# Kernel optimization log

Hardware: AMD Instinct MI355X
Metric: run time of the kernel (lower is better)

The kernel has to match this reference:

```python
import jax, jax.numpy as jnp
import numpy as np

CIN = (512, 1024, 512, 256, 256, 256)
S = (64, 32, 16, 8, 4, 2)
P = 7  # corr_size
B = 8
CH = [P * P + c // 8 for c in CIN]  # lstm state channels per level


def conv3x3(x, w, b):
    y = jax.lax.conv_general_dilated(x, w, (1, 1), ((1, 1), (1, 1)),
                                     dimension_numbers=('NCHW', 'OIHW', 'NCHW'))
    return y + b[None, :, None, None]


def spatial_corr(f1, f2, patch=P):
    # corr[b, di*patch+dj, y, x] = sum_c f1[b,c,y,x] * f2[b,c, y+di-r, x+dj-r]
    r = patch // 2
    Bn, C, H, W = f1.shape
    f2p = jnp.pad(f2, ((0, 0), (0, 0), (r, r), (r, r)))
    outs = [jnp.sum(f1 * f2p[:, :, di:di + H, dj:dj + W], axis=1)
            for di in range(patch) for dj in range(patch)]
    return jnp.stack(outs, axis=1)  # (B, patch*patch, H, W)


def setup_inputs() -> dict:
    key = jax.random.key(0)
    ks = iter(jax.random.split(key, 200))
    d = {}
    for i, (c, s) in enumerate(zip(CIN, S)):
        ch = CH[i]
        d[f'x{i}'] = jax.random.normal(next(ks), (B, c, s, s), jnp.float32)
        d[f'xp{i}'] = jax.random.normal(next(ks), (B, c, s, s), jnp.float32)
        d[f'h{i}'] = jax.random.normal(next(ks), (B, ch, s, s), jnp.float32)
        d[f'c{i}'] = jax.random.normal(next(ks), (B, ch, s, s), jnp.float32)
        d[f'sw{i}'] = jax.random.normal(next(ks), (c // 8, c, 3, 3), jnp.float32) / np.sqrt(c * 9.0)
        d[f'sb{i}'] = jnp.zeros((c // 8,), jnp.float32)
        d[f'lw{i}'] = jax.random.normal(next(ks), (4 * ch, 2 * ch, 3, 3), jnp.float32) / np.sqrt(2 * ch * 9.0)
        d[f'lb{i}'] = jnp.zeros((4 * ch,), jnp.float32)
    return d


def _forward(xs, xps, hs, cs, sws, sbs, lws, lbs):
    h_next, c_next, corrs = [], [], []
    for i in range(len(CIN)):
        summary = jax.nn.relu(conv3x3(xs[i], sws[i], sbs[i]))            # (B, C/8, s, s)
        cf = jax.nn.leaky_relu(spatial_corr(xs[i], xps[i]), 0.01)        # (B, P*P, s, s)
        corrs.append(cf)
        lstm_in = jnp.concatenate([summary, cf, hs[i]], axis=1)          # (B, 2*ch, s, s)
        cx = conv3x3(lstm_in, lws[i], lbs[i])                            # (B, 4*ch, s, s)
        ci, cfg, co, cg = jnp.split(cx, 4, axis=1)
        ig = jax.nn.sigmoid(ci)
        fg = jax.nn.sigmoid(cfg)
        og = jax.nn.sigmoid(co)
        gg = jnp.tanh(cg)
        cn = fg * cs[i] + ig * gg
        hn = og * jnp.tanh(cn)
        h_next.append(hn)
        c_next.append(cn)
    return tuple(h_next + c_next + corrs)


def reference(x0, x1, x2, x3, x4, x5,
              xp0, xp1, xp2, xp3, xp4, xp5,
              h0, h1, h2, h3, h4, h5,
              c0, c1, c2, c3, c4, c5,
              sw0, sw1, sw2, sw3, sw4, sw5,
              sb0, sb1, sb2, sb3, sb4, sb5,
              lw0, lw1, lw2, lw3, lw4, lw5,
              lb0, lb1, lb2, lb3, lb4, lb5):
    xs = [x0, x1, x2, x3, x4, x5]
    xps = [xp0, xp1, xp2, xp3, xp4, xp5]
    hs = [h0, h1, h2, h3, h4, h5]
    cs = [c0, c1, c2, c3, c4, c5]
    sws = [sw0, sw1, sw2, sw3, sw4, sw5]
    sbs = [sb0, sb1, sb2, sb3, sb4, sb5]
    lws = [lw0, lw1, lw2, lw3, lw4, lw5]
    lbs = [lb0, lb1, lb2, lb3, lb4, lb5]
    return _forward(xs, xps, hs, cs, sws, sbs, lws, lbs)
```

## Files before the change

### kernel.cpp

```cpp
#include <hip/hip_runtime.h>
#include <math.h>

typedef _Float16 f16;
typedef _Float16 f16x8 __attribute__((ext_vector_type(8)));
typedef float f32x4 __attribute__((ext_vector_type(4)));

__device__ __forceinline__ float sigmoidf_(float x) { return 1.0f / (1.0f + expf(-x)); }

#define NB 8

__device__ __forceinline__ void decode_swz(int p, int Mtiles, int& mtile, int& nt) {
  if ((Mtiles & 7) == 0) {
    int mch = Mtiles >> 3;
    int c = p & 7, inner = p >> 3;
    nt = inner / mch;
    mtile = c * mch + (inner - nt * mch);
  } else {
    mtile = p % Mtiles;
    nt = p / Mtiles;
  }
}

__global__ void k_nchw2nhwc(const float* __restrict__ in, f16* __restrict__ out,
                            int C, int S, int Cpad, int coff, int Wp, int pad) {
  __shared__ float tile[16][17];
  int xt = blockIdx.x;
  int ct = blockIdx.y;
  int by = blockIdx.z;
  int b = by / S, y = by % S;
  int x0 = xt * 16, c0 = ct * 16;
  int tx = threadIdx.x & 15, tc = threadIdx.x >> 4;
  float v = 0.f;
  if (c0 + tc < C && x0 + tx < S)
    v = in[(((size_t)b * C + c0 + tc) * S + y) * S + x0 + tx];
  tile[tc][tx] = v;
  __syncthreads();
  int tcc = threadIdx.x & 15;
  int txx = threadIdx.x >> 4;
  if (c0 + tcc < C && x0 + txx < S)
    out[(((size_t)b * Wp + y + pad) * Wp + (x0 + txx + pad)) * Cpad + coff + c0 + tcc]
        = (f16)tile[tcc][txx];
}

__global__ void k_wlstm(const float* __restrict__ w, f16* __restrict__ wt,
                        int CH, int CH2, int Jpad, int Cpad) {
  int idx = blockIdx.x * blockDim.x + threadIdx.x;
  int total = 9 * 4 * Jpad * Cpad;
  if (idx >= total) return;
  int ci = idx % Cpad; int t = idx / Cpad;
  int j = t % Jpad; t /= Jpad;
  int g = t % 4; int kk = t / 4;
  float v = 0.f;
  if (j < CH && ci < CH2)
    v = w[((size_t)(g * CH + j) * CH2 + ci) * 9 + kk];
  wt[idx] = (f16)v;
}

__global__ void k_wsum(const float* __restrict__ w, f16* __restrict__ wt,
                       int C8, int C, int Npad, int Cpad) {
  int idx = blockIdx.x * blockDim.x + threadIdx.x;
  int total = 9 * Npad * Cpad;
  if (idx >= total) return;
  int ci = idx % Cpad; int t = idx / Cpad;
  int co = t % Npad; int kk = t / Npad;
  float v = 0.f;
  if (co < C8 && ci < C)
    v = w[((size_t)co * C + ci) * 9 + kk];
  wt[idx] = (f16)v;
}

__global__ void __launch_bounds__(256)
k_conv_gemm(const f16* __restrict__ A,
            const f16* __restrict__ Wt,
            const float* __restrict__ bias,
            f16* __restrict__ D,
            int S, int lS, int CpadX, int CpadL, int C8, int Npad, int M) {
  int w = threadIdx.x >> 6;
  int lane = threadIdx.x & 63;
  int quad = lane >> 4, r = lane & 15;
  int Mtiles = (M + 63) >> 6;
  int mtile, ntile;
  decode_swz(blockIdx.x, Mtiles, mtile, ntile);
  int Sp = S + 2;
  size_t abase[4];
#pragma unroll
  for (int s = 0; s < 4; s++) {
    int m = mtile * 64 + s * 16 + r;
    if (m >= M) m = M - 1;
    int b = m >> (2 * lS);
    int rem = m & ((1 << (2 * lS)) - 1);
    int y = rem >> lS, x = rem & ((1 << lS) - 1);
    abase[s] = (((size_t)b * Sp + y) * Sp + x) * CpadX + quad * 8;
  }
  f32x4 acc[4][4] = {};
  int n0 = ntile * 64;
  int KB = CpadX >> 5;
  int T = 9 * KB;
  int T4 = (T + 3) >> 2;
  int it = w * T4;
  int itEnd = (T < it + T4) ? T : it + T4;
  int nIt = itEnd - it;
  int cb = it / 9;
  int kk = it - cb * 9;

#define CG_LOAD(AF, BF) do { \
    int ky_ = kk / 3, kx_ = kk - 3 * ky_; \
    size_t aoff_ = ((size_t)(ky_ * Sp + kx_)) * CpadX + (size_t)cb * 32; \
    const f16* wp_ = Wt + ((size_t)kk * Npad + n0 + r) * CpadX + quad * 8 + (size_t)cb * 32; \
    _Pragma("unroll") for (int s_ = 0; s_ < 4; s_++) \
      AF[s_] = *(const f16x8*)(A + abase[s_] + aoff_); \
    _Pragma("unroll") for (int t_ = 0; t_ < 4; t_++) \
      BF[t_] = *(const f16x8*)(wp_ + (size_t)t_ * 16 * CpadX); \
  } while (0)
#define CG_ADV() do { kk++; if (kk == 9) { kk = 0; cb++; } } while (0)
#define CG_MF(AF, BF) do { \
    _Pragma("unroll") for (int s_ = 0; s_ < 4; s_++) \
    _Pragma("unroll") for (int t_ = 0; t_ < 4; t_++) \
      acc[s_][t_] = __builtin_amdgcn_mfma_f32_16x16x32_f16(AF[s_], BF[t_], acc[s_][t_], 0, 0, 0); \
  } while (0)

  {
    f16x8 a0[4], b0[4], a1[4], b1[4];
    if (nIt > 0) {
      CG_LOAD(a0, b0); CG_ADV();
      int rem = nIt - 1;
      while (rem >= 2) {
        CG_LOAD(a1, b1); CG_ADV();
        CG_MF(a0, b0);
        CG_LOAD(a0, b0); CG_ADV();
        CG_MF(a1, b1);
        rem -= 2;
      }
      if (rem == 1) { CG_LOAD(a1, b1); CG_MF(a0, b0); CG_MF(a1, b1); }
      else { CG_MF(a0, b0); }
    }
  }
#undef CG_LOAD
#undef CG_ADV
#undef CG_MF

  __shared__ f32x4 red[4][2][4][64];
#pragma unroll
  for (int sh = 0; sh < 2; sh++)
#pragma unroll
    for (int t = 0; t < 4; t++)
      red[w][sh][t][lane] = acc[sh][t];
  __syncthreads();
  f32x4 accR[4];
  if (w < 2) {
#pragma unroll
    for (int t = 0; t < 4; t++)
      accR[t] = red[0][w][t][lane] + red[1][w][t][lane] + red[2][w][t][lane] + red[3][w][t][lane];
  }
  __syncthreads();
#pragma unroll
  for (int sh = 0; sh < 2; sh++)
#pragma unroll
    for (int t = 0; t < 4; t++)
      red[w][sh][t][lane] = acc[2 + sh][t];
  __syncthreads();
  if (w >= 2) {
#pragma unroll
    for (int t = 0; t < 4; t++)
      accR[t] = red[0][w - 2][t][lane] + red[1][w - 2][t][lane] + red[2][w - 2][t][lane] + red[3][w - 2][t][lane];
  }

#pragma unroll
  for (int i = 0; i < 4; i++) {
    int m = mtile * 64 + w * 16 + quad * 4 + i;
    if (m >= M) continue;
    int b = m >> (2 * lS);
    int rem = m & ((1 << (2 * lS)) - 1);
    int y = rem >> lS, x = rem & ((1 << lS) - 1);
    size_t dbase = (((size_t)b * Sp + y + 1) * Sp + (x + 1)) * CpadL;
#pragma unroll
    for (int t = 0; t < 4; t++) {
      int co = n0 + t * 16 + r;
      if (co < C8) {
        float v = accR[t][i] + bias[co];
        D[dbase + co] = (f16)fmaxf(v, 0.f);
      }
    }
  }
}

__global__ void __launch_bounds__(256)
k_lstm_gemm(const f16* __restrict__ A,
            const f16* __restrict__ Wt,
            const float* __restrict__ lb,
            const float* __restrict__ cprev,
            float* __restrict__ hout, float* __restrict__ cout,
            int S, int lS, int CpadL, int CH, int Jpad, int M) {
  int w = threadIdx.x >> 6;
  int lane = threadIdx.x & 63;
  int quad = lane >> 4, r = lane & 15;
  int Mtiles = (M + 63) >> 6;
  int mtile, jt;
  decode_swz(blockIdx.x, Mtiles, mtile, jt);
  int j0 = jt * 16;
  int Sp = S + 2;
  size_t abase[4];
#pragma unroll
  for (int s = 0; s < 4; s++) {
    int m = mtile * 64 + s * 16 + r;
    if (m >= M) m = M - 1;
    int b = m >> (2 * lS);
    int rem = m & ((1 << (2 * lS)) - 1);
    int y = rem >> lS, x = rem & ((1 << lS) - 1);
    abase[s] = (((size_t)b * Sp + y) * Sp + x) * CpadL + quad * 8;
  }
  f32x4 acc[4][4] = {};
  int KB = CpadL >> 5;
  int T = 9 * KB;
  int T4 = (T + 3) >> 2;
  int it = w * T4;
  int itEnd = (T < it + T4) ? T : it + T4;
  int nIt = itEnd - it;
  int cb = it / 9;
  int kk = it - cb * 9;

#define LG_LOAD(AF, BF) do { \
    int ky_ = kk / 3, kx_ = kk - 3 * ky_; \
    size_t aoff_ = ((size_t)(ky_ * Sp + kx_)) * CpadL + (size_t)cb * 32; \
    const f16* wp_ = Wt + (((size_t)kk * 4) * Jpad + j0 + r) * CpadL + quad * 8 + (size_t)cb * 32; \
    _Pragma("unroll") for (int s_ = 0; s_ < 4; s_++) \
      AF[s_] = *(const f16x8*)(A + abase[s_] + aoff_); \
    _Pragma("unroll") for (int g_ = 0; g_ < 4; g_++) \
      BF[g_] = *(const f16x8*)(wp_ + (size_t)g_ * Jpad * CpadL); \
  } while (0)
#define LG_ADV() do { kk++; if (kk == 9) { kk = 0; cb++; } } while (0)
#define LG_MF(AF, BF) do { \
    _Pragma("unroll") for (int s_ = 0; s_ < 4; s_++) \
    _Pragma("unroll") for (int g_ = 0; g_ < 4; g_++) \
      acc[s_][g_] = __builtin_amdgcn_mfma_f32_16x16x32_f16(AF[s_], BF[g_], acc[s_][g_], 0, 0, 0); \
  } while (0)

  {
    f16x8 a0[4], b0[4], a1[4], b1[4];
    if (nIt > 0) {
      LG_LOAD(a0, b0); LG_ADV();
      int rem = nIt - 1;
      while (rem >= 2) {
        LG_LOAD(a1, b1); LG_ADV();
        LG_MF(a0, b0);
        LG_LOAD(a0, b0); LG_ADV();
        LG_MF(a1, b1);
        rem -= 2;
      }
      if (rem == 1) { LG_LOAD(a1, b1); LG_MF(a0, b0); LG_MF(a1, b1); }
      else { LG_MF(a0, b0); }
    }
  }
#undef LG_LOAD
#undef LG_ADV
#undef LG_MF

  __shared__ f32x4 red[4][2][4][64];
#pragma unroll
  for (int sh = 0; sh < 2; sh++)
#pragma unroll
    for (int g = 0; g < 4; g++)
      red[w][sh][g][lane] = acc[sh][g];
  __syncthreads();
  f32x4 accR[4];
  if (w < 2) {
#pragma unroll
    for (int g = 0; g < 4; g++)
      accR[g] = red[0][w][g][lane] + red[1][w][g][lane] + red[2][w][g][lane] + red[3][w][g][lane];
  }
  __syncthreads();
#pragma unroll
  for (int sh = 0; sh < 2; sh++)
#pragma unroll
    for (int g = 0; g < 4; g++)
      red[w][sh][g][lane] = acc[2 + sh][g];
  __syncthreads();
  if (w >= 2) {
#pragma unroll
    for (int g = 0; g < 4; g++)
      accR[g] = red[0][w - 2][g][lane] + red[1][w - 2][g][lane] + red[2][w - 2][g][lane] + red[3][w - 2][g][lane];
  }

  int j = j0 + r;
  if (j >= CH) return;
  float bi = lb[j];
  float bf_ = lb[CH + j];
  float bo = lb[2 * CH + j];
  float bg = lb[3 * CH + j];
#pragma unroll
  for (int i = 0; i < 4; i++) {
    int m = mtile * 64 + w * 16 + quad * 4 + i;
    if (m >= M) continue;
    int b = m >> (2 * lS);
    int rem = m & ((1 << (2 * lS)) - 1);
    int y = rem >> lS, x = rem & ((1 << lS) - 1);
    size_t o = (((size_t)b * CH + j) * S + y) * S + x;
    float ig = sigmoidf_(accR[0][i] + bi);
    float fg = sigmoidf_(accR[1][i] + bf_);
    float og = sigmoidf_(accR[2][i] + bo);
    float gg = tanhf(accR[3][i] + bg);
    float cn = fg * cprev[o] + ig * gg;
    hout[o] = og * tanhf(cn);
    cout[o] = cn;
  }
}

__global__ void k_corr(const float* __restrict__ f1, const float* __restrict__ f2,
                       float* __restrict__ corr_out, f16* __restrict__ D,
                       int C, int S, int CpadL, int C8) {
  int idx = blockIdx.x * blockDim.x + threadIdx.x;
  int total = NB * 49 * S * S;
  if (idx >= total) return;
  int px = idx % S; int t = idx / S;
  int py = t % S; t /= S;
  int d = t % 49; int b = t / 49;
  int qy = py + d / 7 - 3;
  int qx = px + d % 7 - 3;

  float acc = 0.f;
  if (qy >= 0 && qy < S && qx >= 0 && qx < S) {
    const float* p1 = f1 + ((size_t)b * C * S + py) * S + px;
    const float* p2 = f2 + ((size_t)b * C * S + qy) * S + qx;
    size_t cs = (size_t)S * S;
    for (int ci = 0; ci < C; ci++) {
      acc += p1[(size_t)ci * cs] * p2[(size_t)ci * cs];
    }
  }
  float lr = (acc > 0.f) ? acc : 0.01f * acc;
  corr_out[idx] = lr;
  int Sp = S + 2;
  D[(((size_t)b * Sp + py + 1) * Sp + (px + 1)) * CpadL + C8 + d] = (f16)lr;
}

template<int S>
__global__ void __launch_bounds__(256)
k_corr_mfma(const f16* __restrict__ A,
            const f16* __restrict__ A2,
            float* __restrict__ corr_out,
            f16* __restrict__ D,
            int C, int CpadL, int C8) {
  constexpr int XT = S / 16;
  constexpr int Sp = S + 2, Sq = S + 6;
  int nb = gridDim.x;
  int eb = (blockIdx.x % 8) * (nb / 8) + blockIdx.x / 8;
  int wid = eb * 4 + (threadIdx.x >> 6);
  int lane = threadIdx.x & 63;
  int quad = lane >> 4, r = lane & 15;
  int xt = wid % XT; int t1 = wid / XT;
  int y = t1 % S; int b = t1 / S;
  int x0 = xt * 16;

  const f16* pa = A + (((size_t)b * Sp + (y + 1)) * Sp + (x0 + r + 1)) * C + quad * 8;
  int xs1 = x0 + 16 + r; if (xs1 > S + 5) xs1 = S + 5;
  size_t off0 = (size_t)(x0 + r) * C + (size_t)quad * 8;
  size_t off1 = (size_t)xs1 * C + (size_t)quad * 8;
  const f16* pb = A2 + ((size_t)b * Sq + y) * Sq * C;

  f32x4 acc[7][2] = {};
  for (int cb = 0; cb < C; cb += 32) {
    f16x8 af = *(const f16x8*)(pa + cb);
#pragma unroll
    for (int dyo = 0; dyo < 7; dyo++) {
      const f16* pr = pb + (size_t)dyo * Sq * C + cb;
      f16x8 b0 = *(const f16x8*)(pr + off0);
      f16x8 b1 = *(const f16x8*)(pr + off1);
      acc[dyo][0] = __builtin_amdgcn_mfma_f32_16x16x32_f16(af, b0, acc[dyo][0], 0, 0, 0);
      acc[dyo][1] = __builtin_amdgcn_mfma_f32_16x16x32_f16(af, b1, acc[dyo][1], 0, 0, 0);
    }
  }
#pragma unroll
  for (int dyo = 0; dyo < 7; dyo++) {
#pragma unroll
    for (int t = 0; t < 2; t++) {
#pragma unroll
      for (int i = 0; i < 4; i++) {
        int ml = quad * 4 + i;
        int dxo = r - ml + t * 16;
        if (dxo < 0 || dxo > 6) continue;
        float v = acc[dyo][t][i];
        float lr = (v > 0.f) ? v : 0.01f * v;
        int d = dyo * 7 + dxo;
        int x = x0 + ml;
        corr_out[(((size_t)b * 49 + d) * S + y) * S + x] = lr;
        D[(((size_t)b * Sp + y + 1) * Sp + (x + 1)) * CpadL + C8 + d] = (f16)lr;
      }
    }
  }
}

extern "C" void kernel_launch(void* const* d_in, const int* in_sizes, int n_in,
                              void* d_out, int out_size, void* d_ws, size_t ws_size,
                              hipStream_t stream) {
  (void)in_sizes; (void)n_in; (void)out_size; (void)ws_size;
  static const int CINa[6] = {512, 1024, 512, 256, 256, 256};
  static const int Sa[6]   = {64, 32, 16, 8, 4, 2};
  static const int lSa[6]  = {6, 5, 4, 3, 2, 1};
  static const int CHa[6]  = {113, 177, 113, 81, 81, 81};
  static const int CpadLa[6] = {256, 384, 256, 192, 192, 192};
  static const int Jpada[6]  = {128, 192, 128, 96, 96, 96};
  const int B = 8;

  size_t h_off[6], c_off[6], corr_off[6];
  size_t off = 0;
  for (int i = 0; i < 6; i++) { h_off[i] = off;    off += (size_t)B * CHa[i] * Sa[i] * Sa[i]; }
  for (int i = 0; i < 6; i++) { c_off[i] = off;    off += (size_t)B * CHa[i] * Sa[i] * Sa[i]; }
  for (int i = 0; i < 6; i++) { corr_off[i] = off; off += (size_t)B * 49 * Sa[i] * Sa[i]; }

  float* out = (float*)d_out;
  char* ws = (char*)d_ws;
  const size_t offA = 0;
  const size_t offD = 37748736;
  const size_t offWs = offD + 18874368;
  const size_t offWl = offWs + 3145728;
  const size_t offA2 = offWl + 6291456;

  for (int i = 0; i < 6; i++) {
    const float* x  = (const float*)d_in[8 * i + 0];
    const float* xp = (const float*)d_in[8 * i + 1];
    const float* h  = (const float*)d_in[8 * i + 2];
    const float* c  = (const float*)d_in[8 * i + 3];
    const float* sw = (const float*)d_in[8 * i + 4];
    const float* sb = (const float*)d_in[8 * i + 5];
    const float* lw = (const float*)d_in[8 * i + 6];
    const float* lb = (const float*)d_in[8 * i + 7];
    int C = CINa[i], S = Sa[i], lS = lSa[i], CH = CHa[i], C8 = C / 8;
    int CH2 = 2 * CH, CpadL = CpadLa[i], Jpad = Jpada[i];
    int Sp = S + 2;
    int Npad = (C8 + 63) / 64 * 64;
    int M = B * S * S;
    int Mtiles = (M + 63) / 64;

    f16* Abuf = (f16*)(ws + offA);
    f16* Dbuf = (f16*)(ws + offD);
    f16* Wsum = (f16*)(ws + offWs);
    f16* Wlstm = (f16*)(ws + offWl);
    f16* A2buf = (f16*)(ws + offA2);

    size_t sizeA = (size_t)B * Sp * Sp * C * 2;
    size_t sizeD = (size_t)B * Sp * Sp * CpadL * 2;
    hipMemsetAsync(Abuf, 0, sizeA, stream);
    hipMemsetAsync(Dbuf, 0, sizeD, stream);

    {
      dim3 g((S + 15) / 16, (C + 15) / 16, B * S);
      k_nchw2nhwc<<<g, 256, 0, stream>>>(x, Abuf, C, S, C, 0, Sp, 1);
    }
    {
      int tot = 9 * Npad * C;
      k_wsum<<<(tot + 255) / 256, 256, 0, stream>>>(sw, Wsum, C8, C, Npad, C);
    }
    {
      k_conv_gemm<<<Mtiles * (Npad / 64), 256, 0, stream>>>(Abuf, Wsum, sb, Dbuf,
                                                            S, lS, C, CpadL, C8, Npad, M);
    }
    if (i < 3) {
      int Sq = S + 6;
      size_t sizeA2 = (size_t)B * Sq * Sq * C * 2;
      hipMemsetAsync(A2buf, 0, sizeA2, stream);
      {
        dim3 g((S + 15) / 16, (C + 15) / 16, B * S);
        k_nchw2nhwc<<<g, 256, 0, stream>>>(xp, A2buf, C, S, C, 0, Sq, 3);
      }
      int blocks = B * S * (S / 16) / 4;
      if (i == 0)
        k_corr_mfma<64><<<blocks, 256, 0, stream>>>(Abuf, A2buf, out + corr_off[i], Dbuf,
                                                    C, CpadL, C8);
      else if (i == 1)
        k_corr_mfma<32><<<blocks, 256, 0, stream>>>(Abuf, A2buf, out + corr_off[i], Dbuf,
                                                    C, CpadL, C8);
      else
        k_corr_mfma<16><<<blocks, 256, 0, stream>>>(Abuf, A2buf, out + corr_off[i], Dbuf,
                                                    C, CpadL, C8);
    } else {
      int tot = B * 49 * S * S;
      k_corr<<<(tot + 255) / 256, 256, 0, stream>>>(x, xp, out + corr_off[i], Dbuf,
                                                    C, S, CpadL, C8);
    }
    {
      dim3 g((S + 15) / 16, (CH + 15) / 16, B * S);
      k_nchw2nhwc<<<g, 256, 0, stream>>>(h, Dbuf, CH, S, CpadL, C8 + 49, Sp, 1);
    }
    {
      int tot = 9 * 4 * Jpad * CpadL;
      k_wlstm<<<(tot + 255) / 256, 256, 0, stream>>>(lw, Wlstm, CH, CH2, Jpad, CpadL);
    }
    {
      k_lstm_gemm<<<Mtiles * (Jpad / 16), 256, 0, stream>>>(Dbuf, Wlstm, lb, c,
                                                            out + h_off[i], out + c_off[i],
                                                            S, lS, CpadL, CH, Jpad, M);
    }
  }
}
```

Measured before the change: 1.656 ms.

## Use channel-blocked activation and weight layouts, drop split-K reduction in conv GEMMs

Activations move from NHWC to a channel-blocked layout (32-channel blocks, each a padded spatial plane), and weights are repacked into 16x32 tiles, so each MFMA fragment load reads a contiguous chunk. The conv and LSTM GEMMs switch from four waves splitting K with a shared-memory reduction to each wave owning 32 rows of a 128-row M tile over the full K range. This removes the LDS reduction and its barriers. In exchange the grid has half as many blocks per level, which can lower occupancy on the small levels, and each wave now runs the whole K loop alone.

New measurement: 1.682 ms. Within noise of the previous version (+1.5%).

```diff
diff --git a/kernel.cpp b/kernel.cpp
--- a/kernel.cpp
+++ b/kernel.cpp
@@ -37,19 +37,26 @@
   __syncthreads();
   int tcc = threadIdx.x & 15;
   int txx = threadIdx.x >> 4;
-  if (c0 + tcc < C && x0 + txx < S)
-    out[(((size_t)b * Wp + y + pad) * Wp + (x0 + txx + pad)) * Cpad + coff + c0 + tcc]
-        = (f16)tile[tcc][txx];
+  if (c0 + tcc < C && x0 + txx < S) {
+    int c = coff + c0 + tcc;
+    out[((((size_t)b * (Cpad >> 5) + (c >> 5)) * Wp + (y + pad)) * Wp + (x0 + txx + pad)) * 32
+        + (c & 31)] = (f16)tile[tcc][txx];
+  }
 }
 
 __global__ void k_wlstm(const float* __restrict__ w, f16* __restrict__ wt,
                         int CH, int CH2, int Jpad, int Cpad) {
   int idx = blockIdx.x * blockDim.x + threadIdx.x;
-  int total = 9 * 4 * Jpad * Cpad;
+  int JB16 = Jpad >> 4, KBL = Cpad >> 5;
+  int total = 9 * 4 * JB16 * KBL * 512;
   if (idx >= total) return;
-  int ci = idx % Cpad; int t = idx / Cpad;
-  int j = t % Jpad; t /= Jpad;
-  int g = t % 4; int kk = t / 4;
+  int e = idx & 31;
+  int jj = (idx >> 5) & 15;
+  int t = idx >> 9;
+  int cb = t % KBL; t /= KBL;
+  int jb = t % JB16; t /= JB16;
+  int g = t & 3; int kk = t >> 2;
+  int j = jb * 16 + jj, ci = cb * 32 + e;
   float v = 0.f;
   if (j < CH && ci < CH2)
     v = w[((size_t)(g * CH + j) * CH2 + ci) * 9 + kk];
@@ -59,10 +66,15 @@
 __global__ void k_wsum(const float* __restrict__ w, f16* __restrict__ wt,
                        int C8, int C, int Npad, int Cpad) {
   int idx = blockIdx.x * blockDim.x + threadIdx.x;
-  int total = 9 * Npad * Cpad;
+  int NB16 = Npad >> 4, KBX = Cpad >> 5;
+  int total = 9 * NB16 * KBX * 512;
   if (idx >= total) return;
-  int ci = idx % Cpad; int t = idx / Cpad;
-  int co = t % Npad; int kk = t / Npad;
+  int e = idx & 31;
+  int nn = (idx >> 5) & 15;
+  int t = idx >> 9;
+  int cb = t % KBX; t /= KBX;
+  int nb = t % NB16; int kk = t / NB16;
+  int co = nb * 16 + nn, ci = cb * 32 + e;
   float v = 0.f;
   if (co < C8 && ci < C)
     v = w[((size_t)co * C + ci) * 9 + kk];
@@ -78,107 +90,79 @@
   int w = threadIdx.x >> 6;
   int lane = threadIdx.x & 63;
   int quad = lane >> 4, r = lane & 15;
-  int Mtiles = (M + 63) >> 6;
+  int KBX = CpadX >> 5, KBL = CpadL >> 5, NB16 = Npad >> 4;
+  int Mt = (M + 127) >> 7;
   int mtile, ntile;
-  decode_swz(blockIdx.x, Mtiles, mtile, ntile);
+  decode_swz(blockIdx.x, Mt, mtile, ntile);
+  int nb0 = ntile * 4;
   int Sp = S + 2;
-  size_t abase[4];
-#pragma unroll
-  for (int s = 0; s < 4; s++) {
-    int m = mtile * 64 + s * 16 + r;
+  size_t pbase[2];
+#pragma unroll
+  for (int s = 0; s < 2; s++) {
+    int m = mtile * 128 + w * 32 + s * 16 + r;
     if (m >= M) m = M - 1;
     int b = m >> (2 * lS);
     int rem = m & ((1 << (2 * lS)) - 1);
     int y = rem >> lS, x = rem & ((1 << lS) - 1);
-    abase[s] = (((size_t)b * Sp + y) * Sp + x) * CpadX + quad * 8;
-  }
-  f32x4 acc[4][4] = {};
-  int n0 = ntile * 64;
-  int KB = CpadX >> 5;
-  int T = 9 * KB;
-  int T4 = (T + 3) >> 2;
-  int it = w * T4;
-  int itEnd = (T < it + T4) ? T : it + T4;
-  int nIt = itEnd - it;
-  int cb = it / 9;
-  int kk = it - cb * 9;
+    pbase[s] = (((size_t)b * KBX * Sp + y) * Sp + x) * 32 + quad * 8;
+  }
+  size_t wlane = ((size_t)r << 5) + quad * 8;
+  size_t tstep = ((size_t)KBX) << 9;
+  f32x4 acc[2][4] = {};
+  int T = 9 * KBX;
+  int cb = 0, kk = 0;
 
 #define CG_LOAD(AF, BF) do { \
     int ky_ = kk / 3, kx_ = kk - 3 * ky_; \
-    size_t aoff_ = ((size_t)(ky_ * Sp + kx_)) * CpadX + (size_t)cb * 32; \
-    const f16* wp_ = Wt + ((size_t)kk * Npad + n0 + r) * CpadX + quad * 8 + (size_t)cb * 32; \
-    _Pragma("unroll") for (int s_ = 0; s_ < 4; s_++) \
-      AF[s_] = *(const f16x8*)(A + abase[s_] + aoff_); \
+    size_t aoff_ = ((size_t)cb * Sp * Sp + ky_ * Sp + kx_) * 32; \
+    size_t wb_ = (((size_t)(kk * NB16 + nb0) * KBX + cb) << 9) + wlane; \
+    AF[0] = *(const f16x8*)(A + pbase[0] + aoff_); \
+    AF[1] = *(const f16x8*)(A + pbase[1] + aoff_); \
     _Pragma("unroll") for (int t_ = 0; t_ < 4; t_++) \
-      BF[t_] = *(const f16x8*)(wp_ + (size_t)t_ * 16 * CpadX); \
+      BF[t_] = *(const f16x8*)(Wt + wb_ + (size_t)t_ * tstep); \
   } while (0)
 #define CG_ADV() do { kk++; if (kk == 9) { kk = 0; cb++; } } while (0)
 #define CG_MF(AF, BF) do { \
-    _Pragma("unroll") for (int s_ = 0; s_ < 4; s_++) \
+    _Pragma("unroll") for (int s_ = 0; s_ < 2; s_++) \
     _Pragma("unroll") for (int t_ = 0; t_ < 4; t_++) \
       acc[s_][t_] = __builtin_amdgcn_mfma_f32_16x16x32_f16(AF[s_], BF[t_], acc[s_][t_], 0, 0, 0); \
   } while (0)
 
   {
-    f16x8 a0[4], b0[4], a1[4], b1[4];
-    if (nIt > 0) {
+    f16x8 a0[2], b0[4], a1[2], b1[4];
+    CG_LOAD(a0, b0); CG_ADV();
+    int rem = T - 1;
+    while (rem >= 2) {
+      CG_LOAD(a1, b1); CG_ADV();
+      CG_MF(a0, b0);
       CG_LOAD(a0, b0); CG_ADV();
-      int rem = nIt - 1;
-      while (rem >= 2) {
-        CG_LOAD(a1, b1); CG_ADV();
-        CG_MF(a0, b0);
-        CG_LOAD(a0, b0); CG_ADV();
-        CG_MF(a1, b1);
-        rem -= 2;
-      }
-      if (rem == 1) { CG_LOAD(a1, b1); CG_MF(a0, b0); CG_MF(a1, b1); }
-      else { CG_MF(a0, b0); }
-    }
+      CG_MF(a1, b1);
+      rem -= 2;
+    }
+    if (rem == 1) { CG_LOAD(a1, b1); CG_MF(a0, b0); CG_MF(a1, b1); }
+    else { CG_MF(a0, b0); }
   }
 #undef CG_LOAD
 #undef CG_ADV
 #undef CG_MF
 
-  __shared__ f32x4 red[4][2][4][64];
-#pragma unroll
-  for (int sh = 0; sh < 2; sh++)
-#pragma unroll
-    for (int t = 0; t < 4; t++)
-      red[w][sh][t][lane] = acc[sh][t];
-  __syncthreads();
-  f32x4 accR[4];
-  if (w < 2) {
-#pragma unroll
-    for (int t = 0; t < 4; t++)
-      accR[t] = red[0][w][t][lane] + red[1][w][t][lane] + red[2][w][t][lane] + red[3][w][t][lane];
-  }
-  __syncthreads();
-#pragma unroll
-  for (int sh = 0; sh < 2; sh++)
-#pragma unroll
-    for (int t = 0; t < 4; t++)
-      red[w][sh][t][lane] = acc[2 + sh][t];
-  __syncthreads();
-  if (w >= 2) {
-#pragma unroll
-    for (int t = 0; t < 4; t++)
-      accR[t] = red[0][w - 2][t][lane] + red[1][w - 2][t][lane] + red[2][w - 2][t][lane] + red[3][w - 2][t][lane];
-  }
-
-#pragma unroll
-  for (int i = 0; i < 4; i++) {
-    int m = mtile * 64 + w * 16 + quad * 4 + i;
-    if (m >= M) continue;
-    int b = m >> (2 * lS);
-    int rem = m & ((1 << (2 * lS)) - 1);
-    int y = rem >> lS, x = rem & ((1 << lS) - 1);
-    size_t dbase = (((size_t)b * Sp + y + 1) * Sp + (x + 1)) * CpadL;
-#pragma unroll
-    for (int t = 0; t < 4; t++) {
-      int co = n0 + t * 16 + r;
-      if (co < C8) {
-        float v = accR[t][i] + bias[co];
-        D[dbase + co] = (f16)fmaxf(v, 0.f);
+#pragma unroll
+  for (int s = 0; s < 2; s++) {
+#pragma unroll
+    for (int i = 0; i < 4; i++) {
+      int m = mtile * 128 + w * 32 + s * 16 + quad * 4 + i;
+      if (m >= M) continue;
+      int b = m >> (2 * lS);
+      int rem = m & ((1 << (2 * lS)) - 1);
+      int y = rem >> lS, x = rem & ((1 << lS) - 1);
+#pragma unroll
+      for (int t = 0; t < 4; t++) {
+        int co = (nb0 + t) * 16 + r;
+        if (co < C8) {
+          float v = acc[s][t][i] + bias[co];
+          D[((((size_t)b * KBL + (co >> 5)) * Sp + (y + 1)) * Sp + (x + 1)) * 32 + (co & 31)]
+              = (f16)fmaxf(v, 0.f);
+        }
       }
     }
   }
@@ -194,114 +178,85 @@
   int w = threadIdx.x >> 6;
   int lane = threadIdx.x & 63;
   int quad = lane >> 4, r = lane & 15;
-  int Mtiles = (M + 63) >> 6;
+  int KBL = CpadL >> 5, JB16 = Jpad >> 4;
+  int Mt = (M + 127) >> 7;
   int mtile, jt;
-  decode_swz(blockIdx.x, Mtiles, mtile, jt);
-  int j0 = jt * 16;
+  decode_swz(blockIdx.x, Mt, mtile, jt);
   int Sp = S + 2;
-  size_t abase[4];
-#pragma unroll
-  for (int s = 0; s < 4; s++) {
-    int m = mtile * 64 + s * 16 + r;
+  size_t pbase[2];
+#pragma unroll
+  for (int s = 0; s < 2; s++) {
+    int m = mtile * 128 + w * 32 + s * 16 + r;
     if (m >= M) m = M - 1;
     int b = m >> (2 * lS);
     int rem = m & ((1 << (2 * lS)) - 1);
     int y = rem >> lS, x = rem & ((1 << lS) - 1);
-    abase[s] = (((size_t)b * Sp + y) * Sp + x) * CpadL + quad * 8;
-  }
-  f32x4 acc[4][4] = {};
-  int KB = CpadL >> 5;
-  int T = 9 * KB;
-  int T4 = (T + 3) >> 2;
-  int it = w * T4;
-  int itEnd = (T < it + T4) ? T : it + T4;
-  int nIt = itEnd - it;
-  int cb = it / 9;
-  int kk = it - cb * 9;
+    pbase[s] = (((size_t)b * KBL * Sp + y) * Sp + x) * 32 + quad * 8;
+  }
+  size_t wlane = ((size_t)r << 5) + quad * 8;
+  size_t gstep = ((size_t)JB16 * KBL) << 9;
+  f32x4 acc[2][4] = {};
+  int T = 9 * KBL;
+  int cb = 0, kk = 0;
 
 #define LG_LOAD(AF, BF) do { \
     int ky_ = kk / 3, kx_ = kk - 3 * ky_; \
-    size_t aoff_ = ((size_t)(ky_ * Sp + kx_)) * CpadL + (size_t)cb * 32; \
-    const f16* wp_ = Wt + (((size_t)kk * 4) * Jpad + j0 + r) * CpadL + quad * 8 + (size_t)cb * 32; \
-    _Pragma("unroll") for (int s_ = 0; s_ < 4; s_++) \
-      AF[s_] = *(const f16x8*)(A + abase[s_] + aoff_); \
+    size_t aoff_ = ((size_t)cb * Sp * Sp + ky_ * Sp + kx_) * 32; \
+    size_t wb_ = (((size_t)(kk * 4 * JB16 + jt) * KBL + cb) << 9) + wlane; \
+    AF[0] = *(const f16x8*)(A + pbase[0] + aoff_); \
+    AF[1] = *(const f16x8*)(A + pbase[1] + aoff_); \
     _Pragma("unroll") for (int g_ = 0; g_ < 4; g_++) \
-      BF[g_] = *(const f16x8*)(wp_ + (size_t)g_ * Jpad * CpadL); \
+      BF[g_] = *(const f16x8*)(Wt + wb_ + (size_t)g_ * gstep); \
   } while (0)
 #define LG_ADV() do { kk++; if (kk == 9) { kk = 0; cb++; } } while (0)
 #define LG_MF(AF, BF) do { \
-    _Pragma("unroll") for (int s_ = 0; s_ < 4; s_++) \
+    _Pragma("unroll") for (int s_ = 0; s_ < 2; s_++) \
     _Pragma("unroll") for (int g_ = 0; g_ < 4; g_++) \
       acc[s_][g_] = __builtin_amdgcn_mfma_f32_16x16x32_f16(AF[s_], BF[g_], acc[s_][g_], 0, 0, 0); \
   } while (0)
 
   {
-    f16x8 a0[4], b0[4], a1[4], b1[4];
-    if (nIt > 0) {
+    f16x8 a0[2], b0[4], a1[2], b1[4];
+    LG_LOAD(a0, b0); LG_ADV();
+    int rem = T - 1;
+    while (rem >= 2) {
+      LG_LOAD(a1, b1); LG_ADV();
+      LG_MF(a0, b0);
       LG_LOAD(a0, b0); LG_ADV();
-      int rem = nIt - 1;
-      while (rem >= 2) {
-        LG_LOAD(a1, b1); LG_ADV();
-        LG_MF(a0, b0);
-        LG_LOAD(a0, b0); LG_ADV();
-        LG_MF(a1, b1);
-        rem -= 2;
-      }
-      if (rem == 1) { LG_LOAD(a1, b1); LG_MF(a0, b0); LG_MF(a1, b1); }
-      else { LG_MF(a0, b0); }
-    }
+      LG_MF(a1, b1);
+      rem -= 2;
+    }
+    if (rem == 1) { LG_LOAD(a1, b1); LG_MF(a0, b0); LG_MF(a1, b1); }
+    else { LG_MF(a0, b0); }
   }
 #undef LG_LOAD
 #undef LG_ADV
 #undef LG_MF
 
-  __shared__ f32x4 red[4][2][4][64];
-#pragma unroll
-  for (int sh = 0; sh < 2; sh++)
-#pragma unroll
-    for (int g = 0; g < 4; g++)
-      red[w][sh][g][lane] = acc[sh][g];
-  __syncthreads();
-  f32x4 accR[4];
-  if (w < 2) {
-#pragma unroll
-    for (int g = 0; g < 4; g++)
-      accR[g] = red[0][w][g][lane] + red[1][w][g][lane] + red[2][w][g][lane] + red[3][w][g][lane];
-  }
-  __syncthreads();
-#pragma unroll
-  for (int sh = 0; sh < 2; sh++)
-#pragma unroll
-    for (int g = 0; g < 4; g++)
-      red[w][sh][g][lane] = acc[2 + sh][g];
-  __syncthreads();
-  if (w >= 2) {
-#pragma unroll
-    for (int g = 0; g < 4; g++)
-      accR[g] = red[0][w - 2][g][lane] + red[1][w - 2][g][lane] + red[2][w - 2][g][lane] + red[3][w - 2][g][lane];
-  }
-
-  int j = j0 + r;
+  int j = jt * 16 + r;
   if (j >= CH) return;
   float bi = lb[j];
   float bf_ = lb[CH + j];
   float bo = lb[2 * CH + j];
   float bg = lb[3 * CH + j];
 #pragma unroll
-  for (int i = 0; i < 4; i++) {
-    int m = mtile * 64 + w * 16 + quad * 4 + i;
-    if (m >= M) continue;
-    int b = m >> (2 * lS);
-    int rem = m & ((1 << (2 * lS)) - 1);
-    int y = rem >> lS, x = rem & ((1 << lS) - 1);
-    size_t o = (((size_t)b * CH + j) * S + y) * S + x;
-    float ig = sigmoidf_(accR[0][i] + bi);
-    float fg = sigmoidf_(accR[1][i] + bf_);
-    float og = sigmoidf_(accR[2][i] + bo);
-    float gg = tanhf(accR[3][i] + bg);
-    float cn = fg * cprev[o] + ig * gg;
-    hout[o] = og * tanhf(cn);
-    cout[o] = cn;
+  for (int s = 0; s < 2; s++) {
+#pragma unroll
+    for (int i = 0; i < 4; i++) {
+      int m = mtile * 128 + w * 32 + s * 16 + quad * 4 + i;
+      if (m >= M) continue;
+      int b = m >> (2 * lS);
+      int rem = m & ((1 << (2 * lS)) - 1);
+      int y = rem >> lS, x = rem & ((1 << lS) - 1);
+      size_t o = (((size_t)b * CH + j) * S + y) * S + x;
+      float ig = sigmoidf_(acc[s][0][i] + bi);
+      float fg = sigmoidf_(acc[s][1][i] + bf_);
+      float og = sigmoidf_(acc[s][2][i] + bo);
+      float gg = tanhf(acc[s][3][i] + bg);
+      float cn = fg * cprev[o] + ig * gg;
+      hout[o] = og * tanhf(cn);
+      cout[o] = cn;
+    }
   }
 }
 
@@ -329,7 +284,8 @@
   float lr = (acc > 0.f) ? acc : 0.01f * acc;
   corr_out[idx] = lr;
   int Sp = S + 2;
-  D[(((size_t)b * Sp + py + 1) * Sp + (px + 1)) * CpadL + C8 + d] = (f16)lr;
+  int ch = C8 + d, KBL = CpadL >> 5;
+  D[((((size_t)b * KBL + (ch >> 5)) * Sp + (py + 1)) * Sp + (px + 1)) * 32 + (ch & 31)] = (f16)lr;
 }
 
 template<int S>
@@ -341,6 +297,7 @@
             int C, int CpadL, int C8) {
   constexpr int XT = S / 16;
   constexpr int Sp = S + 2, Sq = S + 6;
+  int KBX = C >> 5, KBL = CpadL >> 5;
   int nb = gridDim.x;
   int eb = (blockIdx.x % 8) * (nb / 8) + blockIdx.x / 8;
   int wid = eb * 4 + (threadIdx.x >> 6);
@@ -350,18 +307,21 @@
   int y = t1 % S; int b = t1 / S;
   int x0 = xt * 16;
 
-  const f16* pa = A + (((size_t)b * Sp + (y + 1)) * Sp + (x0 + r + 1)) * C + quad * 8;
+  size_t baseA = ((((size_t)b * KBX) * Sp + (y + 1)) * Sp + (x0 + r + 1)) * 32 + quad * 8;
+  size_t stepA = (size_t)Sp * Sp * 32;
   int xs1 = x0 + 16 + r; if (xs1 > S + 5) xs1 = S + 5;
-  size_t off0 = (size_t)(x0 + r) * C + (size_t)quad * 8;
-  size_t off1 = (size_t)xs1 * C + (size_t)quad * 8;
-  const f16* pb = A2 + ((size_t)b * Sq + y) * Sq * C;
+  size_t off0 = (size_t)(x0 + r) * 32 + quad * 8;
+  size_t off1 = (size_t)xs1 * 32 + quad * 8;
+  size_t baseB = ((size_t)b * KBX) * Sq * Sq * 32 + (size_t)y * Sq * 32;
+  size_t stepB = (size_t)Sq * Sq * 32;
 
   f32x4 acc[7][2] = {};
-  for (int cb = 0; cb < C; cb += 32) {
-    f16x8 af = *(const f16x8*)(pa + cb);
+  for (int cbi = 0; cbi < KBX; cbi++) {
+    f16x8 af = *(const f16x8*)(A + baseA + (size_t)cbi * stepA);
+    const f16* pbb = A2 + baseB + (size_t)cbi * stepB;
 #pragma unroll
     for (int dyo = 0; dyo < 7; dyo++) {
-      const f16* pr = pb + (size_t)dyo * Sq * C + cb;
+      const f16* pr = pbb + (size_t)dyo * Sq * 32;
       f16x8 b0 = *(const f16x8*)(pr + off0);
       f16x8 b1 = *(const f16x8*)(pr + off1);
       acc[dyo][0] = __builtin_amdgcn_mfma_f32_16x16x32_f16(af, b0, acc[dyo][0], 0, 0, 0);
@@ -382,7 +342,9 @@
         int d = dyo * 7 + dxo;
         int x = x0 + ml;
         corr_out[(((size_t)b * 49 + d) * S + y) * S + x] = lr;
-        D[(((size_t)b * Sp + y + 1) * Sp + (x + 1)) * CpadL + C8 + d] = (f16)lr;
+        int ch = C8 + d;
+        D[((((size_t)b * KBL + (ch >> 5)) * Sp + (y + 1)) * Sp + (x + 1)) * 32 + (ch & 31)]
+            = (f16)lr;
       }
     }
   }
@@ -428,7 +390,7 @@
     int Sp = S + 2;
     int Npad = (C8 + 63) / 64 * 64;
     int M = B * S * S;
-    int Mtiles = (M + 63) / 64;
+    int Mt128 = (M + 127) / 128;
 
     f16* Abuf = (f16*)(ws + offA);
     f16* Dbuf = (f16*)(ws + offD);
@@ -450,8 +412,8 @@
       k_wsum<<<(tot + 255) / 256, 256, 0, stream>>>(sw, Wsum, C8, C, Npad, C);
     }
     {
-      k_conv_gemm<<<Mtiles * (Npad / 64), 256, 0, stream>>>(Abuf, Wsum, sb, Dbuf,
-                                                            S, lS, C, CpadL, C8, Npad, M);
+      k_conv_gemm<<<Mt128 * (Npad / 64), 256, 0, stream>>>(Abuf, Wsum, sb, Dbuf,
+                                                           S, lS, C, CpadL, C8, Npad, M);
     }
     if (i < 3) {
       int Sq = S + 6;
@@ -485,9 +447,9 @@
       k_wlstm<<<(tot + 255) / 256, 256, 0, stream>>>(lw, Wlstm, CH, CH2, Jpad, CpadL);
     }
     {
-      k_lstm_gemm<<<Mtiles * (Jpad / 16), 256, 0, stream>>>(Dbuf, Wlstm, lb, c,
-                                                            out + h_off[i], out + c_off[i],
-                                                            S, lS, CpadL, CH, Jpad, M);
-    }
-  }
-}
+      k_lstm_gemm<<<Mt128 * (Jpad / 16), 256, 0, stream>>>(Dbuf, Wlstm, lb, c,
+                                                           out + h_off[i], out + c_off[i],
+                                                           S, lS, CpadL, CH, Jpad, M);
+    }
+  }
+}
```
